# Performance work log

Hardware: AMD Instinct MI355X
Metric: run time of the kernel (lower is better)

## Reference

```python
import jax, jax.numpy as jnp
import numpy as np

IN_DIM = 128
OUT_DIM = 128
NUM_HEADS = 4
HEAD_DIM = OUT_DIM // NUM_HEADS
TEMP = 0.2
NEG_SLOPE = 0.2


def _xavier(key, shape, gain=1.414):
    fan_in, fan_out = shape[-2], shape[-1]
    limit = gain * np.sqrt(6.0 / (fan_in + fan_out))
    return jax.random.uniform(key, shape, jnp.float32, -limit, limit)


def setup_inputs() -> dict:
    key = jax.random.key(0)
    k_h, k_W, k_a, k_mw, k_mb = jax.random.split(key, 5)
    B, N = 4, 2048
    h = jax.random.normal(k_h, (B, N, IN_DIM), jnp.float32)
    W = _xavier(k_W, (NUM_HEADS, IN_DIM, HEAD_DIM))
    a = _xavier(k_a, (NUM_HEADS, 2 * HEAD_DIM, 1))
    merge_w = _xavier(k_mw, (OUT_DIM, OUT_DIM))  # nn.Linear weight [out, in]
    merge_b = jnp.zeros((OUT_DIM,), jnp.float32)
    return {"h": h, "W": W, "a": a, "merge_w": merge_w, "merge_b": merge_b}


def reference(h, W, a, merge_w, merge_b):
    B, N, _ = h.shape
    # Wh: [B, H, N, head_dim]
    Wh = jnp.einsum('bni,hio->bhno', h, W)
    a_sq = a[..., 0]                                  # [H, 2*hd]
    a_src, a_dst = a_sq[:, :HEAD_DIM], a_sq[:, HEAD_DIM:]
    # additive score decomposition avoids the NxNx2hd concat blowup
    s_src = jnp.einsum('bhno,ho->bhn', Wh, a_src)     # contribution of node i (row)
    s_dst = jnp.einsum('bhno,ho->bhn', Wh, a_dst)     # contribution of node j (col)
    e = s_src[:, :, :, None] + s_dst[:, :, None, :]   # [B, H, N, N]
    e = jnp.where(e > 0, e, NEG_SLOPE * e)            # LeakyReLU(0.2)
    alpha = jax.nn.softmax(e / TEMP, axis=3)          # softmax over neighbors j
    h_prime_heads = jnp.einsum('bhnm,bhmo->bhno', alpha, Wh)
    h_concat = h_prime_heads.transpose(0, 2, 1, 3).reshape(B, N, OUT_DIM)
    h_prime = h_concat @ merge_w.T + merge_b
    return h_prime, alpha.mean(axis=1)
```

## Files before the change

### kernel.cpp

```cpp
#include <hip/hip_runtime.h>
#include <stddef.h>

#define NN 2048
#define DIN 128
#define HD 32

typedef __attribute__((ext_vector_type(8))) short short8;
typedef __attribute__((ext_vector_type(4))) float f32x4;

constexpr float SLOPE = 0.2f;
constexpr float LC = 7.2134752044448170f;

__device__ __forceinline__ unsigned int pack_rne(float a, float b){
    unsigned int xa = __float_as_uint(a), xb = __float_as_uint(b);
    unsigned int ra = (xa + 0x7fffu + ((xa >> 16) & 1u)) >> 16;
    unsigned int rb = (xb + 0x7fffu + ((xb >> 16) & 1u)) >> 16;
    return ra | (rb << 16);
}

__global__ __launch_bounds__(256) void kWhScore(const float* __restrict__ hg,
                                                const float* __restrict__ Wg,
                                                const float* __restrict__ ag,
                                                unsigned short* __restrict__ whT,
                                                float* __restrict__ sSrc,
                                                float* __restrict__ sDst,
                                                float* __restrict__ maxPart)
{
    __shared__ float Hl[32][132];
    __shared__ float wal[8][128];
    __shared__ float al[256];
    const int t = threadIdx.x;
    const int b = blockIdx.x >> 6;
    const int tile = blockIdx.x & 63;
    const int n0 = tile*32;
    #pragma unroll
    for (int ii = 0; ii < 4; ++ii){
        const int idx = t + 256*ii;
        const int r = idx >> 5, c4 = idx & 31;
        *(float4*)&Hl[r][c4*4] = *(const float4*)&hg[((size_t)b*NN + n0 + r)*DIN + c4*4];
    }
    al[t] = ag[t];
    __syncthreads();
    #pragma unroll
    for (int jj = 0; jj < 4; ++jj){
        const int idx = t + 256*jj;
        const int combo = idx >> 7, i = idx & 127;
        const int hh = combo >> 1, d = combo & 1;
        const float* wrow = &Wg[hh*4096 + i*32];
        const float* av = &al[hh*64 + d*32];
        float s = 0.f;
        #pragma unroll
        for (int q = 0; q < 8; ++q){
            const float4 w = *(const float4*)&wrow[q*4];
            s += w.x*av[q*4] + w.y*av[q*4+1] + w.z*av[q*4+2] + w.w*av[q*4+3];
        }
        wal[combo][i] = s;
    }
    __syncthreads();
    {
        const int combo = t >> 5, nl = t & 31;
        const int hh = combo >> 1, d = combo & 1;
        float s = 0.f;
        #pragma unroll
        for (int q = 0; q < 32; ++q){
            const float4 hv = *(const float4*)&Hl[nl][q*4];
            const float4 wv = *(const float4*)&wal[combo][q*4];
            s += hv.x*wv.x + hv.y*wv.y + hv.z*wv.z + hv.w*wv.w;
        }
        const int bh = b*4 + hh;
        if (d == 0) sSrc[bh*NN + n0 + nl] = s;
        else {
            sDst[bh*NN + n0 + nl] = s;
            float lm = s;
            #pragma unroll
            for (int off = 1; off < 32; off <<= 1) lm = fmaxf(lm, __shfl_xor(lm, off));
            if (nl == 0) maxPart[bh*64 + tile] = lm;
        }
    }
    const int og = t >> 5, nl = t & 31;
    const int o0 = og*4;
    float acc[16];
    #pragma unroll
    for (int k = 0; k < 16; ++k) acc[k] = 0.f;
    for (int kc = 0; kc < 16; ++kc){
        const float4 hA = *(const float4*)&Hl[nl][kc*8];
        const float4 hB = *(const float4*)&Hl[nl][kc*8+4];
        const float hreg[8] = {hA.x,hA.y,hA.z,hA.w,hB.x,hB.y,hB.z,hB.w};
        #pragma unroll
        for (int hh = 0; hh < 4; ++hh){
            #pragma unroll
            for (int i8 = 0; i8 < 8; ++i8){
                const float4 w = *(const float4*)&Wg[hh*4096 + (kc*8+i8)*32 + o0];
                acc[hh*4+0] = fmaf(hreg[i8], w.x, acc[hh*4+0]);
                acc[hh*4+1] = fmaf(hreg[i8], w.y, acc[hh*4+1]);
                acc[hh*4+2] = fmaf(hreg[i8], w.z, acc[hh*4+2]);
                acc[hh*4+3] = fmaf(hreg[i8], w.w, acc[hh*4+3]);
            }
        }
    }
    #pragma unroll
    for (int hh = 0; hh < 4; ++hh){
        #pragma unroll
        for (int j = 0; j < 4; ++j){
            const unsigned int x = __float_as_uint(acc[hh*4+j]);
            whT[((size_t)(b*4+hh)*32 + o0 + j)*NN + n0 + nl] =
                (unsigned short)((x + 0x7fffu + ((x>>16)&1u)) >> 16);
        }
    }
}

__global__ void kMaxR(const float* __restrict__ maxPart, float* __restrict__ maxFull){
    const int t = threadIdx.x;
    if (t < 16){
        float m = maxPart[t*64];
        for (int i = 1; i < 64; ++i) m = fmaxf(m, maxPart[t*64+i]);
        maxFull[t] = m;
    }
}

__global__ __launch_bounds__(256) void kAttnM(const unsigned short* __restrict__ whT,
                                              const float* __restrict__ sSrc,
                                              const float* __restrict__ sDst,
                                              const float* __restrict__ maxFull,
                                              float* __restrict__ invZ,
                                              unsigned short* __restrict__ hcb)
{
    __shared__ unsigned short WtT[32][136];
    __shared__ float sdl[128];
    const int t = threadIdx.x;
    const int wv = t >> 6, lane = t & 63;
    const int q = lane >> 4, c = lane & 15;
    const int bh = blockIdx.x >> 5;
    const int n0 = (blockIdx.x & 31)*64 + wv*16;
    const int b = bh >> 2, hh = bh & 3;
    const float mx = maxFull[bh];
    const float ssrc = sSrc[bh*NN + n0 + c];
    const float q0 = ssrc + mx;
    const float R = fmaxf(q0, SLOPE*q0) * LC;
    const float a1 = ssrc*LC - R;
    const float a2 = SLOPE*LC*ssrc - R;
    f32x4 acc0 = {0.f,0.f,0.f,0.f}, acc1 = {0.f,0.f,0.f,0.f};
    float Zp = 0.f;
    for (int mt = 0; mt < 16; ++mt){
        const int mb = mt*128;
        __syncthreads();
        #pragma unroll
        for (int ps = 0; ps < 2; ++ps){
            const int o = ps*16 + (t >> 4);
            const int mo = (t & 15)*8;
            *(short8*)&WtT[o][mo] = *(const short8*)&whT[((size_t)bh*32 + o)*NN + mb + mo];
        }
        if (t < 128) sdl[t] = LC * sDst[bh*NN + mb + t];
        __syncthreads();
        #pragma unroll
        for (int ks = 0; ks < 4; ++ks){
            const int m8 = ks*32 + q*8;
            float p[8];
            #pragma unroll
            for (int j = 0; j < 8; ++j){
                const float u = sdl[m8 + j];
                p[j] = exp2f(fmaxf(a1 + u, fmaf(SLOPE, u, a2)));
                Zp += p[j];
            }
            short8 aF;
            #pragma unroll
            for (int j = 0; j < 8; j += 2){
                ((unsigned int*)&aF)[j>>1] = (__float_as_uint(p[j]) >> 16)
                                           | (__float_as_uint(p[j+1]) & 0xffff0000u);
            }
            const short8 bF0 = *(const short8*)&WtT[c][m8];
            const short8 bF1 = *(const short8*)&WtT[16 + c][m8];
            acc0 = __builtin_amdgcn_mfma_f32_16x16x32_bf16(aF, bF0, acc0, 0, 0, 0);
            acc1 = __builtin_amdgcn_mfma_f32_16x16x32_bf16(aF, bF1, acc1, 0, 0, 0);
        }
    }
    Zp += __shfl_xor(Zp, 16);
    Zp += __shfl_xor(Zp, 32);
    const float iz = 1.0f / Zp;
    if (q == 0) invZ[bh*NN + n0 + c] = iz;
    #pragma unroll
    for (int reg = 0; reg < 4; ++reg){
        const int row = q*4 + reg;
        const float izr = __shfl(iz, row);
        const size_t base = ((size_t)b*NN + n0 + row)*128 + hh*32;
        hcb[base + c]      = (unsigned short)((pack_rne(acc0[reg]*izr, 0.f)) & 0xffffu);
        hcb[base + 16 + c] = (unsigned short)((pack_rne(acc1[reg]*izr, 0.f)) & 0xffffu);
    }
}

__global__ __launch_bounds__(256) void kAlpha(const float* __restrict__ sSrc,
                                              const float* __restrict__ sDst,
                                              const float* __restrict__ maxFull,
                                              const float* __restrict__ invZ,
                                              float* __restrict__ out1)
{
    __shared__ float sdl[4][NN];
    const int t = threadIdx.x;
    const int b = blockIdx.x >> 9;
    const int n0 = (blockIdx.x & 511) * 4;
    for (int i = t; i < 4*NN; i += 256)
        sdl[i >> 11][i & (NN-1)] = LC * sDst[(size_t)(b*4 + (i>>11))*NN + (i & (NN-1))];
    __syncthreads();
    float a1[4][4], a2[4][4], cf[4][4];
    #pragma unroll
    for (int hh = 0; hh < 4; ++hh){
        const float mx = maxFull[b*4+hh];
        #pragma unroll
        for (int rr = 0; rr < 4; ++rr){
            const int bhn = (b*4+hh)*NN + n0 + rr;
            const float ss = sSrc[bhn];
            const float q0 = ss + mx;
            const float R = fmaxf(q0, SLOPE*q0)*LC;
            a1[rr][hh] = ss*LC - R;
            a2[rr][hh] = SLOPE*LC*ss - R;
            cf[rr][hh] = 0.25f * invZ[bhn];
        }
    }
    for (int mb = 0; mb < NN; mb += 256){
        const int m = mb + t;
        const float u0 = sdl[0][m], u1 = sdl[1][m], u2 = sdl[2][m], u3 = sdl[3][m];
        #pragma unroll
        for (int rr = 0; rr < 4; ++rr){
            float v;
            v  = cf[rr][0]*exp2f(fmaxf(a1[rr][0]+u0, fmaf(SLOPE, u0, a2[rr][0])));
            v += cf[rr][1]*exp2f(fmaxf(a1[rr][1]+u1, fmaf(SLOPE, u1, a2[rr][1])));
            v += cf[rr][2]*exp2f(fmaxf(a1[rr][2]+u2, fmaf(SLOPE, u2, a2[rr][2])));
            v += cf[rr][3]*exp2f(fmaxf(a1[rr][3]+u3, fmaf(SLOPE, u3, a2[rr][3])));
            out1[((size_t)b*NN + n0 + rr)*NN + m] = v;
        }
    }
}

__global__ __launch_bounds__(256) void kMergeM(const unsigned short* __restrict__ hcb,
                                               const float* __restrict__ mw,
                                               const float* __restrict__ mbv,
                                               float* __restrict__ out0)
{
    __shared__ unsigned short mwb[128][136];
    const int t = threadIdx.x;
    const int wv = t >> 6, lane = t & 63;
    const int q = lane >> 4, c = lane & 15;
    for (int i = t; i < 128*64; i += 256){
        const int j = i >> 6, k2 = i & 63;
        const float2 v = *(const float2*)&mw[j*128 + k2*2];
        *(unsigned int*)&mwb[j][k2*2] = pack_rne(v.x, v.y);
    }
    __syncthreads();
    const int row0 = blockIdx.x*64 + wv*16;
    f32x4 acc[8];
    #pragma unroll
    for (int ot = 0; ot < 8; ++ot) acc[ot] = (f32x4){0.f,0.f,0.f,0.f};
    #pragma unroll
    for (int ks = 0; ks < 4; ++ks){
        const short8 aF = *(const short8*)&hcb[((size_t)row0 + c)*128 + ks*32 + q*8];
        #pragma unroll
        for (int ot = 0; ot < 8; ++ot){
            const short8 bF = *(const short8*)&mwb[ot*16 + c][ks*32 + q*8];
            acc[ot] = __builtin_amdgcn_mfma_f32_16x16x32_bf16(aF, bF, acc[ot], 0, 0, 0);
        }
    }
    #pragma unroll
    for (int ot = 0; ot < 8; ++ot){
        const int col = ot*16 + c;
        const float bias = mbv[col];
        #pragma unroll
        for (int reg = 0; reg < 4; ++reg){
            const size_t row = (size_t)row0 + q*4 + reg;
            out0[row*128 + col] = acc[ot][reg] + bias;
        }
    }
}

extern "C" void kernel_launch(void* const* d_in, const int* in_sizes, int n_in,
                              void* d_out, int out_size, void* d_ws, size_t ws_size,
                              hipStream_t stream)
{
    const float* hg  = (const float*)d_in[0];
    const float* Wg  = (const float*)d_in[1];
    const float* ag  = (const float*)d_in[2];
    const float* mw  = (const float*)d_in[3];
    const float* mbv = (const float*)d_in[4];
    float* out0 = (float*)d_out;
    float* out1 = out0 + (size_t)4*NN*128;

    float* ws      = (float*)d_ws;
    float* sSrc    = ws;
    float* sDst    = sSrc + 32768;
    float* maxPart = sDst + 32768;
    float* maxFull = maxPart + 1024;
    float* invZ    = maxFull + 16;
    unsigned short* whT = (unsigned short*)(invZ + 32768);
    unsigned short* hcb = whT + (size_t)16*32*NN;

    hipLaunchKernelGGL(kWhScore, dim3(256),  dim3(256), 0, stream, hg, Wg, ag, whT, sSrc, sDst, maxPart);
    hipLaunchKernelGGL(kMaxR,    dim3(1),    dim3(64),  0, stream, maxPart, maxFull);
    hipLaunchKernelGGL(kAttnM,   dim3(512),  dim3(256), 0, stream, whT, sSrc, sDst, maxFull, invZ, hcb);
    hipLaunchKernelGGL(kAlpha,   dim3(2048), dim3(256), 0, stream, sSrc, sDst, maxFull, invZ, out1);
    hipLaunchKernelGGL(kMergeM,  dim3(128),  dim3(256), 0, stream, hcb, mw, mbv, out0);
}
```

Measured before the change: 169.5 us.

## Fold max reduction into consumers and fuse alpha with merge projection

Removes the single-block max-reduction kernel: each consumer block now reduces the 64 partial maxima itself. The alpha-mean kernel and the merge linear layer become one kernel with 512 blocks of 16 rows each, so the launch count drops from five to three. Each block now also converts the merge weights to bf16 into shared memory (512 times instead of 128) and does a small MFMA tile. The alpha loop is reorganised so each wave handles 4 rows across 64 columns, giving narrower coalesced stores per row, and the larger shared footprint may reduce occupancy.

```diff
diff --git a/kernel.cpp b/kernel.cpp
--- a/kernel.cpp
+++ b/kernel.cpp
@@ -109,19 +109,10 @@
     }
 }
 
-__global__ void kMaxR(const float* __restrict__ maxPart, float* __restrict__ maxFull){
-    const int t = threadIdx.x;
-    if (t < 16){
-        float m = maxPart[t*64];
-        for (int i = 1; i < 64; ++i) m = fmaxf(m, maxPart[t*64+i]);
-        maxFull[t] = m;
-    }
-}
-
 __global__ __launch_bounds__(256) void kAttnM(const unsigned short* __restrict__ whT,
                                               const float* __restrict__ sSrc,
                                               const float* __restrict__ sDst,
-                                              const float* __restrict__ maxFull,
+                                              const float* __restrict__ maxPart,
                                               float* __restrict__ invZ,
                                               unsigned short* __restrict__ hcb)
 {
@@ -133,7 +124,9 @@
     const int bh = blockIdx.x >> 5;
     const int n0 = (blockIdx.x & 31)*64 + wv*16;
     const int b = bh >> 2, hh = bh & 3;
-    const float mx = maxFull[bh];
+    float mx = maxPart[bh*64];
+    #pragma unroll 8
+    for (int i = 1; i < 64; ++i) mx = fmaxf(mx, maxPart[bh*64 + i]);
     const float ssrc = sSrc[bh*NN + n0 + c];
     const float q0 = ssrc + mx;
     const float R = fmaxf(q0, SLOPE*q0) * LC;
@@ -188,26 +181,39 @@
     }
 }
 
-__global__ __launch_bounds__(256) void kAlpha(const float* __restrict__ sSrc,
-                                              const float* __restrict__ sDst,
-                                              const float* __restrict__ maxFull,
-                                              const float* __restrict__ invZ,
-                                              float* __restrict__ out1)
+__global__ __launch_bounds__(256) void kAlphaMerge(const float* __restrict__ sSrc,
+                                                   const float* __restrict__ sDst,
+                                                   const float* __restrict__ maxPart,
+                                                   const float* __restrict__ invZ,
+                                                   const unsigned short* __restrict__ hcb,
+                                                   const float* __restrict__ mw,
+                                                   const float* __restrict__ mbv,
+                                                   float* __restrict__ out1,
+                                                   float* __restrict__ out0)
 {
     __shared__ float sdl[4][NN];
+    __shared__ unsigned short mwb[128][136];
     const int t = threadIdx.x;
-    const int b = blockIdx.x >> 9;
-    const int n0 = (blockIdx.x & 511) * 4;
+    const int wv = t >> 6, lane = t & 63;
+    const int b = blockIdx.x >> 7;
+    const int n0 = (blockIdx.x & 127) * 16;
     for (int i = t; i < 4*NN; i += 256)
         sdl[i >> 11][i & (NN-1)] = LC * sDst[(size_t)(b*4 + (i>>11))*NN + (i & (NN-1))];
+    for (int i = t; i < 128*64; i += 256){
+        const int j = i >> 6, k2 = i & 63;
+        const float2 v = *(const float2*)&mw[j*128 + k2*2];
+        *(unsigned int*)&mwb[j][k2*2] = pack_rne(v.x, v.y);
+    }
     __syncthreads();
     float a1[4][4], a2[4][4], cf[4][4];
     #pragma unroll
     for (int hh = 0; hh < 4; ++hh){
-        const float mx = maxFull[b*4+hh];
+        float mx = maxPart[(b*4+hh)*64];
+        #pragma unroll 8
+        for (int i = 1; i < 64; ++i) mx = fmaxf(mx, maxPart[(b*4+hh)*64 + i]);
         #pragma unroll
         for (int rr = 0; rr < 4; ++rr){
-            const int bhn = (b*4+hh)*NN + n0 + rr;
+            const int bhn = (b*4+hh)*NN + n0 + wv*4 + rr;
             const float ss = sSrc[bhn];
             const float q0 = ss + mx;
             const float R = fmaxf(q0, SLOPE*q0)*LC;
@@ -216,8 +222,8 @@
             cf[rr][hh] = 0.25f * invZ[bhn];
         }
     }
-    for (int mb = 0; mb < NN; mb += 256){
-        const int m = mb + t;
+    for (int mb = 0; mb < NN; mb += 64){
+        const int m = mb + lane;
         const float u0 = sdl[0][m], u1 = sdl[1][m], u2 = sdl[2][m], u3 = sdl[3][m];
         #pragma unroll
         for (int rr = 0; rr < 4; ++rr){
@@ -226,48 +232,30 @@
             v += cf[rr][1]*exp2f(fmaxf(a1[rr][1]+u1, fmaf(SLOPE, u1, a2[rr][1])));
             v += cf[rr][2]*exp2f(fmaxf(a1[rr][2]+u2, fmaf(SLOPE, u2, a2[rr][2])));
             v += cf[rr][3]*exp2f(fmaxf(a1[rr][3]+u3, fmaf(SLOPE, u3, a2[rr][3])));
-            out1[((size_t)b*NN + n0 + rr)*NN + m] = v;
-        }
-    }
-}
-
-__global__ __launch_bounds__(256) void kMergeM(const unsigned short* __restrict__ hcb,
-                                               const float* __restrict__ mw,
-                                               const float* __restrict__ mbv,
-                                               float* __restrict__ out0)
-{
-    __shared__ unsigned short mwb[128][136];
-    const int t = threadIdx.x;
-    const int wv = t >> 6, lane = t & 63;
+            out1[((size_t)b*NN + n0 + wv*4 + rr)*NN + m] = v;
+        }
+    }
     const int q = lane >> 4, c = lane & 15;
-    for (int i = t; i < 128*64; i += 256){
-        const int j = i >> 6, k2 = i & 63;
-        const float2 v = *(const float2*)&mw[j*128 + k2*2];
-        *(unsigned int*)&mwb[j][k2*2] = pack_rne(v.x, v.y);
-    }
-    __syncthreads();
-    const int row0 = blockIdx.x*64 + wv*16;
-    f32x4 acc[8];
-    #pragma unroll
-    for (int ot = 0; ot < 8; ++ot) acc[ot] = (f32x4){0.f,0.f,0.f,0.f};
+    const size_t row0 = (size_t)b*NN + n0;
+    f32x4 macc[2];
+    macc[0] = (f32x4){0.f,0.f,0.f,0.f};
+    macc[1] = (f32x4){0.f,0.f,0.f,0.f};
     #pragma unroll
     for (int ks = 0; ks < 4; ++ks){
-        const short8 aF = *(const short8*)&hcb[((size_t)row0 + c)*128 + ks*32 + q*8];
-        #pragma unroll
-        for (int ot = 0; ot < 8; ++ot){
-            const short8 bF = *(const short8*)&mwb[ot*16 + c][ks*32 + q*8];
-            acc[ot] = __builtin_amdgcn_mfma_f32_16x16x32_bf16(aF, bF, acc[ot], 0, 0, 0);
-        }
-    }
-    #pragma unroll
-    for (int ot = 0; ot < 8; ++ot){
-        const int col = ot*16 + c;
+        const short8 aF = *(const short8*)&hcb[(row0 + c)*128 + ks*32 + q*8];
+        #pragma unroll
+        for (int j = 0; j < 2; ++j){
+            const short8 bF = *(const short8*)&mwb[(wv*2+j)*16 + c][ks*32 + q*8];
+            macc[j] = __builtin_amdgcn_mfma_f32_16x16x32_bf16(aF, bF, macc[j], 0, 0, 0);
+        }
+    }
+    #pragma unroll
+    for (int j = 0; j < 2; ++j){
+        const int col = (wv*2+j)*16 + c;
         const float bias = mbv[col];
         #pragma unroll
-        for (int reg = 0; reg < 4; ++reg){
-            const size_t row = (size_t)row0 + q*4 + reg;
-            out0[row*128 + col] = acc[ot][reg] + bias;
-        }
+        for (int reg = 0; reg < 4; ++reg)
+            out0[(row0 + q*4 + reg)*128 + col] = macc[j][reg] + bias;
     }
 }
 
@@ -287,14 +275,11 @@
     float* sSrc    = ws;
     float* sDst    = sSrc + 32768;
     float* maxPart = sDst + 32768;
-    float* maxFull = maxPart + 1024;
-    float* invZ    = maxFull + 16;
+    float* invZ    = maxPart + 1024;
     unsigned short* whT = (unsigned short*)(invZ + 32768);
     unsigned short* hcb = whT + (size_t)16*32*NN;
 
-    hipLaunchKernelGGL(kWhScore, dim3(256),  dim3(256), 0, stream, hg, Wg, ag, whT, sSrc, sDst, maxPart);
-    hipLaunchKernelGGL(kMaxR,    dim3(1),    dim3(64),  0, stream, maxPart, maxFull);
-    hipLaunchKernelGGL(kAttnM,   dim3(512),  dim3(256), 0, stream, whT, sSrc, sDst, maxFull, invZ, hcb);
-    hipLaunchKernelGGL(kAlpha,   dim3(2048), dim3(256), 0, stream, sSrc, sDst, maxFull, invZ, out1);
-    hipLaunchKernelGGL(kMergeM,  dim3(128),  dim3(256), 0, stream, hcb, mw, mbv, out0);
-}
+    hipLaunchKernelGGL(kWhScore,   dim3(256), dim3(256), 0, stream, hg, Wg, ag, whT, sSrc, sDst, maxPart);
+    hipLaunchKernelGGL(kAttnM,     dim3(512), dim3(256), 0, stream, whT, sSrc, sDst, maxPart, invZ, hcb);
+    hipLaunchKernelGGL(kAlphaMerge,dim3(512), dim3(256), 0, stream, sSrc, sDst, maxPart, invZ, hcb, mw, mbv, out1, out0);
+}
```

Result: slower. 173.9 us (+2.6%).
